# Optimization experiments

Measured on AMD Instinct MI355X. Metric: run time of the kernel, lower is better.

Reference implementation:

```python
import jax, jax.numpy as jnp
import numpy as np
from jax import lax

B, N, C = 4, 16384, 384
HEADS, HD = 8, 48
ALPHA = 4.0
KS = 5
HH = WW = 128


def setup_inputs() -> dict:
    key = jax.random.key(0)
    ks = jax.random.split(key, 9)
    s = 0.02
    return {
        "x": jax.random.normal(ks[0], (B, N, C), jnp.float32),
        "W_qg": jax.random.normal(ks[1], (C, 2 * C), jnp.float32) * s,
        "W_kv": jax.random.normal(ks[2], (C, 2 * C), jnp.float32) * s,
        "W_proj": jax.random.normal(ks[3], (C, C), jnp.float32) * s,
        "b_proj": jnp.zeros((C,), jnp.float32),
        "pos_enc": jax.random.normal(ks[4], (1, N, C), jnp.float32) * 0.02,
        "power_p": jax.random.normal(ks[5], (1, HEADS, 1, HD), jnp.float32) * 0.5,
        "scale_p": jax.random.normal(ks[6], (1, 1, C), jnp.float32) * 0.5,
        "dwc_w": jax.random.normal(ks[7], (HD, 1, KS, KS), jnp.float32) * s,
        "dwc_b": jnp.zeros((HD,), jnp.float32),
        "H": HH,
        "W": WW,
    }


def _relu_pow(x, p):
    # relu(x) ** p with safe gradients at x <= 0
    r = jax.nn.relu(x)
    base = jnp.where(r > 0, r, 1.0)
    return jnp.where(r > 0, base ** p, 0.0)


def reference(x, W_qg, W_kv, W_proj, b_proj, pos_enc, power_p, scale_p, dwc_w, dwc_b, H, W):
    Bx, Nx, Cx = x.shape
    h = power_p.shape[1]
    hd = power_p.shape[-1]

    qg = x @ W_qg                      # [B,N,2C]
    q, g = qg[..., :Cx], qg[..., Cx:]
    kv = x @ W_kv                      # [B,N,2C] (sr_ratio == 1)
    k, v = kv[..., :Cx], kv[..., Cx:]
    n = Nx
    k = k + pos_enc

    scale = jax.nn.softplus(scale_p)            # [1,1,C]
    power = 1.0 + ALPHA * jax.nn.sigmoid(power_p)  # [1,h,1,hd]
    q = q / scale
    k = k / scale

    # [B,h,N,hd]
    q = q.reshape(Bx, Nx, h, hd).transpose(0, 2, 1, 3)
    k = k.reshape(Bx, n, h, hd).transpose(0, 2, 1, 3)
    v = v.reshape(Bx, n, h, hd).transpose(0, 2, 1, 3)

    q_pos = _relu_pow(q, power)
    q_neg = _relu_pow(-q, power)
    k_pos = _relu_pow(k, power)
    k_neg = _relu_pow(-k, power)

    q_sim = jnp.concatenate([q_pos, q_neg], axis=-1)   # [B,h,N,2hd]
    q_opp = jnp.concatenate([q_neg, q_pos], axis=-1)
    kk = jnp.concatenate([k_pos, k_neg], axis=-1)      # [B,h,n,2hd]
    v1, v2 = v[..., : hd // 2], v[..., hd // 2:]

    k_mean = kk.mean(axis=2, keepdims=True)            # [B,h,1,2hd]
    inv_n = 1.0 / n

    z_sim = 1.0 / (jnp.sum(q_sim * k_mean, axis=-1, keepdims=True) + 1e-6)
    kv1 = jnp.einsum('bhnd,bhne->bhde', kk, v1) * inv_n  # [B,h,2hd,hd/2]
    x_sim = jnp.einsum('bhnd,bhde->bhne', q_sim, kv1) * z_sim

    z_opp = 1.0 / (jnp.sum(q_opp * k_mean, axis=-1, keepdims=True) + 1e-6)
    kv2 = jnp.einsum('bhnd,bhne->bhde', kk, v2) * inv_n
    x_opp = jnp.einsum('bhnd,bhde->bhne', q_opp, kv2) * z_opp

    out = jnp.concatenate([x_sim, x_opp], axis=-1)     # [B,h,N,hd]
    out = out.transpose(0, 2, 1, 3).reshape(Bx, Nx, Cx)

    # depthwise conv gate on v
    v4 = v.reshape(Bx * h, H, W, hd).transpose(0, 3, 1, 2)  # [B*h, hd, H, W]
    vc = lax.conv_general_dilated(
        v4, dwc_w, window_strides=(1, 1), padding='SAME',
        feature_group_count=hd,
        dimension_numbers=('NCHW', 'OIHW', 'NCHW'))
    vc = vc + dwc_b[None, :, None, None]
    v_out = vc.reshape(Bx, Cx, Nx).transpose(0, 2, 1)  # [B,N,C]

    out = (out + v_out) * g
    out = out @ W_proj + b_proj
    return out
```

## Files before the change

### kernel.cpp

```cpp
#include <hip/hip_runtime.h>
#include <math.h>


#define NB 4
#define NTOK 16384
#define CDIM 384
#define NHEAD 8
#define HDIM 48
#define IMGH 128
#define IMGW 128

typedef unsigned short u16;
typedef unsigned int u32;
typedef __attribute__((ext_vector_type(8))) short bf16x8;
typedef __attribute__((ext_vector_type(4))) float f32x4;

__device__ __forceinline__ float bf2f(u16 u) {
  return __uint_as_float(((unsigned)u) << 16);
}
__device__ __forceinline__ u16 f2bf(float f) {
  unsigned u = __float_as_uint(f);
  u += 0x7FFF + ((u >> 16) & 1);
  return (u16)(u >> 16);
}
__device__ __forceinline__ float pow_mag(float r, float p) {
  if (r < 1e-20f) return 0.0f;
  return exp2f(fminf(p * log2f(r), 80.0f));
}
__device__ __forceinline__ float ldx1(const void* p, size_t i, bool f32) {
  return f32 ? ((const float*)p)[i] : bf2f(((const u16*)p)[i]);
}
__device__ __forceinline__ void gload16(u16* lds, const u16* g) {
  __builtin_amdgcn_global_load_lds(
      (const __attribute__((address_space(1))) u32*)g,
      (__attribute__((address_space(3))) u32*)lds, 16, 0, 0);
}

__global__ __launch_bounds__(256) void k0_detect(const void* __restrict__ x,
                                                 int* __restrict__ flag) {
  __shared__ int s[256];
  const u16* p = (const u16*)x;
  const int t = threadIdx.x;
  int good = 0;
#pragma unroll
  for (int i = 0; i < 16; ++i) {
    const u16 w = p[t * 16 + i];
    const int e = (w >> 7) & 0xFF;
    good += (e >= 0x60 && e <= 0x85) ? 1 : 0;
  }
  s[t] = good;
  __syncthreads();
  for (int o = 128; o > 0; o >>= 1) {
    if (t < o) s[t] += s[t + o];
    __syncthreads();
  }
  if (t == 0) *flag = (s[0] >= (4096 * 4) / 5) ? 0 : 1;
}

__global__ __launch_bounds__(256) void kx_convert(const void* __restrict__ x,
                                                  const int* __restrict__ flag,
                                                  u16* __restrict__ xbf) {
  if (*flag == 0) return;
  const size_t S = (size_t)NB * NTOK * CDIM;
  const size_t tid = (size_t)blockIdx.x * 256 + threadIdx.x;
  const size_t stride = (size_t)gridDim.x * 256;
  const float4* xf = (const float4*)x;
  for (size_t i = tid; i < S / 8; i += stride) {
    const float4 a = xf[i * 2 + 0];
    const float4 b = xf[i * 2 + 1];
    *(ushort4*)(xbf + i * 8 + 0) = make_ushort4(f2bf(a.x), f2bf(a.y), f2bf(a.z), f2bf(a.w));
    *(ushort4*)(xbf + i * 8 + 4) = make_ushort4(f2bf(b.x), f2bf(b.y), f2bf(b.z), f2bf(b.w));
  }
}

__global__ __launch_bounds__(256) void kprep(
    const void* __restrict__ Wqg, const void* __restrict__ Wkv,
    const void* __restrict__ Wp, const int* __restrict__ flag,
    u16* __restrict__ W2T, u16* __restrict__ WpT)
{
  const bool f32 = (*flag != 0);
  const int idx = blockIdx.x * 256 + threadIdx.x;
  if (idx < 1536 * 384) {
    const int n = idx / 384, k = idx - n * 384;
    const float v = (n < 768) ? ldx1(Wqg, (size_t)k * 768 + n, f32)
                              : ldx1(Wkv, (size_t)k * 768 + (n - 768), f32);
    W2T[idx] = f2bf(v);
  } else {
    const int j = idx - 1536 * 384;
    if (j < 384 * 384) {
      const int n = j / 384, k = j - n * 384;
      WpT[j] = f2bf(ldx1(Wp, (size_t)k * 384 + n, f32));
    }
  }
}

__global__ __launch_bounds__(512) void k1_mfma(
    const void* __restrict__ x, const u16* __restrict__ xbf,
    const u16* __restrict__ W2T,
    const void* __restrict__ pos_enc, const void* __restrict__ scale_p,
    const int* __restrict__ flag, const int conv_ok,
    u16* __restrict__ qsT, u16* __restrict__ gT, u16* __restrict__ ksT, u16* __restrict__ vT)
{
  const bool f32 = (*flag != 0);
  const bool fast = (!f32) || (conv_ok != 0);
  const u16* Asrc = f32 ? xbf : (const u16*)x;
  __shared__ __align__(16) u16 smem[17408];
  u16* Asm = smem;
  u16* Bsm = smem + 8192;
  const int t = threadIdx.x;
  const int bid = blockIdx.x;
  const int rm = (bid & 7) * 768 + (bid >> 3);
  const int m_idx = rm / 12;
  const int n_idx = rm - m_idx * 12;
  const int n0 = n_idx * 128;
  const int m0 = m_idx * 128;
  const int wave = t >> 6, lane = t & 63;
  const int wr = wave >> 2, wc = wave & 3;
  const int lm = lane & 15, lq = lane >> 4;

  f32x4 acc[4][2] = {};

  auto STAGE = [&](int k0) {
#pragma unroll
    for (int i = 0; i < 2; ++i) {
      const int chunk = i * 512 + t;
      const int row = chunk >> 3, c8 = chunk & 7;
      const int sc8 = c8 ^ (row & 7);
      u16* lpA = &Asm[(i * 512 + wave * 64) * 8];
      u16* lpB = &Bsm[(i * 512 + wave * 64) * 8];
      gload16(lpA, Asrc + (size_t)(m0 + row) * CDIM + k0 + sc8 * 8);
      gload16(lpB, W2T + (size_t)(n0 + row) * CDIM + k0 + sc8 * 8);
    }
  };
  auto COMPUTE = [&]() {
#pragma unroll
    for (int kh = 0; kh < 2; ++kh) {
      bf16x8 af[4], bfr[2];
#pragma unroll
      for (int r = 0; r < 4; ++r) {
        const int row = wr * 64 + r * 16 + lm;
        af[r] = *(const bf16x8*)&Asm[row * 64 + (((kh * 4 + lq) ^ (row & 7)) * 8)];
      }
#pragma unroll
      for (int cb = 0; cb < 2; ++cb) {
        const int row = wc * 32 + cb * 16 + lm;
        bfr[cb] = *(const bf16x8*)&Bsm[row * 64 + (((kh * 4 + lq) ^ (row & 7)) * 8)];
      }
#pragma unroll
      for (int r = 0; r < 4; ++r)
#pragma unroll
        for (int cb = 0; cb < 2; ++cb)
          acc[r][cb] = __builtin_amdgcn_mfma_f32_16x16x32_bf16(af[r], bfr[cb], acc[r][cb], 0, 0, 0);
    }
  };

  if (fast) {
    for (int ks = 0; ks < 6; ++ks) {
      STAGE(ks * 64);
      __syncthreads();
      COMPUTE();
      __syncthreads();
    }
  } else {
    for (int k0 = 0; k0 < CDIM; k0 += 64) {
#pragma unroll
      for (int i = 0; i < 2; ++i) {
        const int chunk = t + i * 512;
        const int row = chunk >> 3, c8 = chunk & 7;
        const int ldsoff = row * 64 + ((c8 ^ (row & 7)) * 8);
        const float* xp = (const float*)x + (size_t)(m0 + row) * CDIM + k0 + c8 * 8;
        const float4 v0 = *(const float4*)xp;
        const float4 v1 = *(const float4*)(xp + 4);
        *(ushort4*)&Asm[ldsoff]     = make_ushort4(f2bf(v0.x), f2bf(v0.y), f2bf(v0.z), f2bf(v0.w));
        *(ushort4*)&Asm[ldsoff + 4] = make_ushort4(f2bf(v1.x), f2bf(v1.y), f2bf(v1.z), f2bf(v1.w));
        *(uint4*)&Bsm[ldsoff] = *(const uint4*)(W2T + (size_t)(n0 + row) * CDIM + k0 + c8 * 8);
      }
      __syncthreads();
      COMPUTE();
      __syncthreads();
    }
  }

  u16* et = smem;
  const int b = m0 >> 14;
  const int TOK0 = m0 & (NTOK - 1);
  const int region = n0 / CDIM;
#pragma unroll
  for (int cb = 0; cb < 2; ++cb) {
    const int cl = wc * 32 + cb * 16 + lm;
    const int c = (n0 - region * CDIM) + cl;
    float inv = 1.0f;
    if (region == 0 || region == 2) inv = 1.0f / log1pf(expf(ldx1(scale_p, c, f32)));
#pragma unroll
    for (int r = 0; r < 4; ++r) {
      const int tl = wr * 64 + r * 16 + lq * 4;
      const f32x4 v = acc[r][cb];
      ushort4 w;
      if (region == 2) {
        const int tok = TOK0 + tl;
        const float p0 = ldx1(pos_enc, (size_t)(tok + 0) * CDIM + c, f32);
        const float p1 = ldx1(pos_enc, (size_t)(tok + 1) * CDIM + c, f32);
        const float p2 = ldx1(pos_enc, (size_t)(tok + 2) * CDIM + c, f32);
        const float p3 = ldx1(pos_enc, (size_t)(tok + 3) * CDIM + c, f32);
        w = make_ushort4(f2bf((v[0] + p0) * inv), f2bf((v[1] + p1) * inv),
                         f2bf((v[2] + p2) * inv), f2bf((v[3] + p3) * inv));
      } else if (region == 0) {
        w = make_ushort4(f2bf(v[0] * inv), f2bf(v[1] * inv), f2bf(v[2] * inv), f2bf(v[3] * inv));
      } else {
        w = make_ushort4(f2bf(v[0]), f2bf(v[1]), f2bf(v[2]), f2bf(v[3]));
      }
      *(ushort4*)&et[cl * 136 + tl] = w;
    }
  }
  __syncthreads();
  u16* dst = (region == 0) ? qsT : (region == 1) ? gT : (region == 2) ? ksT : vT;
  const int cbase = b * CDIM + (n0 - region * CDIM);
#pragma unroll
  for (int i = 0; i < 4; ++i) {
    const int idx = i * 512 + t;
    const int row = idx >> 4, seg = idx & 15;
    const uint4 val = *(const uint4*)&et[row * 136 + seg * 8];
    *(uint4*)(dst + ((size_t)(cbase + row)) * NTOK + TOK0 + seg * 8) = val;
  }
}

__global__ __launch_bounds__(256) void k2_stats(
    const u16* __restrict__ ksT, const u16* __restrict__ vT,
    const void* __restrict__ power_p, const int* __restrict__ flag,
    float* __restrict__ km, float* __restrict__ kvm)
{
  const bool f32 = (*flag != 0);
  __shared__ float kkL[96][65];
  __shared__ float vL[48][65];
  __shared__ float pw[48];
  const int bh = blockIdx.x;
  const int b = bh >> 3, h = bh & 7;
  const int t = threadIdx.x;
  if (t < 48) pw[t] = 1.0f + 4.0f / (1.0f + expf(-ldx1(power_p, h * HDIM + t, f32)));
  __syncthreads();
  const int td = t & 15, te = t >> 4;
  float acc[6][3] = {};
  float ksum = 0.0f;
  const u16* ksbase = ksT + ((size_t)(b * CDIM + h * HDIM)) * NTOK;
  const u16* vbase  = vT  + ((size_t)(b * CDIM + h * HDIM)) * NTOK;
  const int n0base = blockIdx.y * 1024;
  for (int tile = 0; tile < 16; ++tile) {
    const int n0 = n0base + tile * 64;
    for (int i = t; i < 48 * 16; i += 256) {
      const int c = i >> 4, qd = (i & 15) * 4;
      ushort4 kq = *(const ushort4*)(ksbase + (size_t)c * NTOK + n0 + qd);
      ushort4 vq = *(const ushort4*)(vbase  + (size_t)c * NTOK + n0 + qd);
      const float p = pw[c];
      float kf[4] = {bf2f(kq.x), bf2f(kq.y), bf2f(kq.z), bf2f(kq.w)};
      float vf[4] = {bf2f(vq.x), bf2f(vq.y), bf2f(vq.z), bf2f(vq.w)};
#pragma unroll
      for (int jj = 0; jj < 4; ++jj) {
        const float f = pow_mag(fabsf(kf[jj]), p);
        kkL[c][qd + jj]      = (kf[jj] > 0.f) ? f : 0.f;
        kkL[c + 48][qd + jj] = (kf[jj] < 0.f) ? f : 0.f;
        vL[c][qd + jj] = vf[jj];
      }
    }
    __syncthreads();
#pragma unroll 2
    for (int nn = 0; nn < 64; ++nn) {
      float av[6], bv[3];
#pragma unroll
      for (int i = 0; i < 6; ++i) av[i] = kkL[td * 6 + i][nn];
#pragma unroll
      for (int j = 0; j < 3; ++j) bv[j] = vL[te * 3 + j][nn];
#pragma unroll
      for (int i = 0; i < 6; ++i)
#pragma unroll
        for (int j = 0; j < 3; ++j)
          acc[i][j] = fmaf(av[i], bv[j], acc[i][j]);
    }
    if (t < 96) {
#pragma unroll 4
      for (int nn = 0; nn < 64; ++nn) ksum += kkL[t][nn];
    }
    __syncthreads();
  }
  const float inv_n = 1.0f / (float)NTOK;
#pragma unroll
  for (int i = 0; i < 6; ++i)
#pragma unroll
    for (int j = 0; j < 3; ++j)
      atomicAdd(&kvm[(size_t)bh * 96 * 48 + (td * 6 + i) * 48 + (te * 3 + j)], acc[i][j] * inv_n);
  if (t < 96) atomicAdd(&km[bh * 96 + t], ksum * inv_n);
}

__global__ __launch_bounds__(256) void k3_attn(
    const u16* __restrict__ qsT, u16* __restrict__ attnT,
    const float* __restrict__ km_g, const float* __restrict__ kvm_g,
    const void* __restrict__ power_p, const int* __restrict__ flag)
{
  const bool f32 = (*flag != 0);
  __shared__ __align__(16) float kvmL[96][48];
  __shared__ float kmL[96];
  __shared__ float pw[48];
  const int bh = blockIdx.y;
  const int b = bh >> 3, h = bh & 7;
  const int t = threadIdx.x;
  for (int i = t; i < 96 * 48; i += 256) kvmL[i / 48][i % 48] = kvm_g[(size_t)bh * 96 * 48 + i];
  if (t < 96) kmL[t] = km_g[bh * 96 + t];
  if (t < 48) pw[t] = 1.0f + 4.0f / (1.0f + expf(-ldx1(power_p, h * HDIM + t, f32)));
  __syncthreads();
  const int n = blockIdx.x * 512 + t;
  const size_t chan0 = ((size_t)(b * CDIM + h * HDIM)) * NTOK + n;
  const u16* qbase = qsT + chan0;
  u16* obase = attnT + chan0;
  float4 accs[2][6] = {}, acco[2][6] = {};
  float zs[2] = {}, zo[2] = {};
  for (int d = 0; d < 48; ++d) {
    const float p = pw[d];
    float qp[2], qn[2];
#pragma unroll
    for (int i = 0; i < 2; ++i) {
      const float qv = bf2f(qbase[(size_t)d * NTOK + i * 256]);
      const float f = pow_mag(fabsf(qv), p);
      qp[i] = (qv > 0.f) ? f : 0.f;
      qn[i] = (qv < 0.f) ? f : 0.f;
      zs[i] = fmaf(qp[i], kmL[d], zs[i]); zs[i] = fmaf(qn[i], kmL[d + 48], zs[i]);
      zo[i] = fmaf(qn[i], kmL[d], zo[i]); zo[i] = fmaf(qp[i], kmL[d + 48], zo[i]);
    }
#pragma unroll
    for (int e4 = 0; e4 < 6; ++e4) {
      const float4 kvA = *(const float4*)&kvmL[d][e4 * 4];
      const float4 kvB = *(const float4*)&kvmL[d + 48][e4 * 4];
      const float4 kvC = *(const float4*)&kvmL[d][24 + e4 * 4];
      const float4 kvD = *(const float4*)&kvmL[d + 48][24 + e4 * 4];
#pragma unroll
      for (int i = 0; i < 2; ++i) {
        accs[i][e4].x = fmaf(qp[i], kvA.x, fmaf(qn[i], kvB.x, accs[i][e4].x));
        accs[i][e4].y = fmaf(qp[i], kvA.y, fmaf(qn[i], kvB.y, accs[i][e4].y));
        accs[i][e4].z = fmaf(qp[i], kvA.z, fmaf(qn[i], kvB.z, accs[i][e4].z));
        accs[i][e4].w = fmaf(qp[i], kvA.w, fmaf(qn[i], kvB.w, accs[i][e4].w));
        acco[i][e4].x = fmaf(qn[i], kvC.x, fmaf(qp[i], kvD.x, acco[i][e4].x));
        acco[i][e4].y = fmaf(qn[i], kvC.y, fmaf(qp[i], kvD.y, acco[i][e4].y));
        acco[i][e4].z = fmaf(qn[i], kvC.z, fmaf(qp[i], kvD.z, acco[i][e4].z));
        acco[i][e4].w = fmaf(qn[i], kvC.w, fmaf(qp[i], kvD.w, acco[i][e4].w));
      }
    }
  }
#pragma unroll
  for (int i = 0; i < 2; ++i) {
    const float zsi = 1.0f / (zs[i] + 1e-6f);
    const float zoi = 1.0f / (zo[i] + 1e-6f);
#pragma unroll
    for (int e4 = 0; e4 < 6; ++e4) {
      const float4 s = accs[i][e4], o = acco[i][e4];
      obase[(size_t)(e4 * 4 + 0) * NTOK + i * 256]    = f2bf(s.x * zsi);
      obase[(size_t)(e4 * 4 + 1) * NTOK + i * 256]    = f2bf(s.y * zsi);
      obase[(size_t)(e4 * 4 + 2) * NTOK + i * 256]    = f2bf(s.z * zsi);
      obase[(size_t)(e4 * 4 + 3) * NTOK + i * 256]    = f2bf(s.w * zsi);
      obase[(size_t)(24 + e4 * 4 + 0) * NTOK + i * 256] = f2bf(o.x * zoi);
      obase[(size_t)(24 + e4 * 4 + 1) * NTOK + i * 256] = f2bf(o.y * zoi);
      obase[(size_t)(24 + e4 * 4 + 2) * NTOK + i * 256] = f2bf(o.z * zoi);
      obase[(size_t)(24 + e4 * 4 + 3) * NTOK + i * 256] = f2bf(o.w * zoi);
    }
  }
}

__global__ __launch_bounds__(256) void k4_conv_combine(
    const u16* __restrict__ vT, const u16* __restrict__ gT,
    const void* __restrict__ dwc_w, const void* __restrict__ dwc_b,
    const int* __restrict__ flag,
    u16* __restrict__ attnT)
{
  const bool f32 = (*flag != 0);
  __shared__ float tile[20][128];
  const int bc = blockIdx.y;
  const int y0 = blockIdx.x * 16;
  const int t = threadIdx.x;
  const int d = bc % 48;
  float w[25];
#pragma unroll
  for (int i = 0; i < 25; ++i) w[i] = ldx1(dwc_w, d * 25 + i, f32);
  const float bias = ldx1(dwc_b, d, f32);
  const u16* vimg = vT + (size_t)bc * NTOK;
  for (int i = t; i < 20 * 128; i += 256) {
    const int r = i >> 7, xx = i & 127;
    const int gy = y0 + r - 2;
    tile[r][xx] = (gy >= 0 && gy < IMGH) ? bf2f(vimg[gy * IMGW + xx]) : 0.f;
  }
  __syncthreads();
  u16* abase = attnT + (size_t)bc * NTOK;
  const u16* gbase = gT + (size_t)bc * NTOK;
#pragma unroll
  for (int k = 0; k < 8; ++k) {
    const int px = t + k * 256;
    const int yy = px >> 7, xcol = px & 127;
    float acc = bias;
#pragma unroll
    for (int dy = 0; dy < 5; ++dy)
#pragma unroll
      for (int dx = 0; dx < 5; ++dx) {
        const int ux = xcol + dx - 2;
        const float val = (ux >= 0 && ux < IMGW) ? tile[yy + dy][ux] : 0.f;
        acc = fmaf(w[dy * 5 + dx], val, acc);
      }
    const int gidx = (y0 + yy) * IMGW + xcol;
    abase[gidx] = f2bf((bf2f(abase[gidx]) + acc) * bf2f(gbase[gidx]));
  }
}

__global__ __launch_bounds__(256) void k4b_transpose(
    const u16* __restrict__ src,
    u16* __restrict__ dst)
{
  __shared__ u16 tile[64][68];
  const int b  = blockIdx.z;
  const int c0 = blockIdx.y * 64;
  const int n0 = blockIdx.x * 64;
  const int t = threadIdx.x;
  const int tr = t >> 4, tq = t & 15;
#pragma unroll
  for (int i = 0; i < 4; ++i) {
    const int r = tr + i * 16;
    *(ushort4*)&tile[r][tq * 4] =
        *(const ushort4*)(src + ((size_t)(b * CDIM + c0 + r)) * NTOK + n0 + tq * 4);
  }
  __syncthreads();
#pragma unroll
  for (int i = 0; i < 4; ++i) {
    const int n = tr + i * 16;
    const ushort4 vv = make_ushort4(tile[tq * 4 + 0][n], tile[tq * 4 + 1][n],
                                    tile[tq * 4 + 2][n], tile[tq * 4 + 3][n]);
    *(ushort4*)(dst + ((size_t)(b * NTOK + n0 + n)) * CDIM + c0 + tq * 4) = vv;
  }
}

__global__ __launch_bounds__(256) void k5_mfma(
    const u16* __restrict__ A,
    const u16* __restrict__ WpT,
    const void* __restrict__ bp, const int* __restrict__ flag,
    void* __restrict__ out)
{
  const bool f32 = (*flag != 0);
  __shared__ __align__(16) u16 Asm[128 * 64];
  __shared__ __align__(16) u16 Bsm[128 * 64];
  const int t = threadIdx.x;
  const int bid = blockIdx.x;
  const int rm = (bid & 7) * 192 + (bid >> 3);
  const int m_idx = rm / 3;
  const int n_idx = rm - m_idx * 3;
  const int n0 = n_idx * 128;
  const int m0 = m_idx * 128;
  const int wave = t >> 6, lane = t & 63;
  const int wr = wave >> 1, wc = wave & 1;
  const int lm = lane & 15, lq = lane >> 4;

  f32x4 acc[4][4] = {};

  auto STAGE = [&](int k0) {
#pragma unroll
    for (int i = 0; i < 4; ++i) {
      const int chunk = i * 256 + t;
      const int row = chunk >> 3, c8 = chunk & 7;
      const int sc8 = c8 ^ (row & 7);
      u16* lpA = &Asm[(i * 256 + wave * 64) * 8];
      u16* lpB = &Bsm[(i * 256 + wave * 64) * 8];
      gload16(lpA, A + (size_t)(m0 + row) * CDIM + k0 + sc8 * 8);
      gload16(lpB, WpT + (size_t)(n0 + row) * CDIM + k0 + sc8 * 8);
    }
  };
  auto COMPUTE = [&]() {
#pragma unroll
    for (int kh = 0; kh < 2; ++kh) {
      bf16x8 af[4], bfr[4];
#pragma unroll
      for (int r = 0; r < 4; ++r) {
        const int row = wr * 64 + r * 16 + lm;
        af[r] = *(const bf16x8*)&Asm[row * 64 + (((kh * 4 + lq) ^ (row & 7)) * 8)];
      }
#pragma unroll
      for (int cb = 0; cb < 4; ++cb) {
        const int row = wc * 64 + cb * 16 + lm;
        bfr[cb] = *(const bf16x8*)&Bsm[row * 64 + (((kh * 4 + lq) ^ (row & 7)) * 8)];
      }
#pragma unroll
      for (int r = 0; r < 4; ++r)
#pragma unroll
        for (int cb = 0; cb < 4; ++cb)
          acc[r][cb] = __builtin_amdgcn_mfma_f32_16x16x32_bf16(af[r], bfr[cb], acc[r][cb], 0, 0, 0);
    }
  };

  for (int ks = 0; ks < 6; ++ks) {
    STAGE(ks * 64);
    __syncthreads();
    COMPUTE();
    __syncthreads();
  }

#pragma unroll
  for (int cb = 0; cb < 4; ++cb) {
    const int cg = n0 + wc * 64 + cb * 16 + lm;
    const float bb = ldx1(bp, cg, f32);
#pragma unroll
    for (int r = 0; r < 4; ++r) {
      const int rowtok = m0 + wr * 64 + r * 16 + lq * 4;
      const f32x4 v = acc[r][cb];
#pragma unroll
      for (int reg = 0; reg < 4; ++reg) {
        const size_t o = (size_t)(rowtok + reg) * CDIM + cg;
        if (f32) ((float*)out)[o] = v[reg] + bb;
        else     ((u16*)out)[o]   = f2bf(v[reg] + bb);
      }
    }
  }
}

extern "C" void kernel_launch(void* const* d_in, const int* in_sizes, int n_in,
                              void* d_out, int out_size, void* d_ws, size_t ws_size,
                              hipStream_t stream) {
  const void* x       = d_in[0];
  const void* Wqg     = d_in[1];
  const void* Wkv     = d_in[2];
  const void* Wproj   = d_in[3];
  const void* bproj   = d_in[4];
  const void* pos_enc = d_in[5];
  const void* power_p = d_in[6];
  const void* scale_p = d_in[7];
  const void* dwc_w   = d_in[8];
  const void* dwc_b   = d_in[9];

  const size_t S = (size_t)NB * NTOK * CDIM;
  const size_t stats_off   = 256;
  const size_t stats_bytes = (size_t)(32 * 96 + 32 * 96 * 48) * sizeof(float);
  const size_t w2t_elems = 1536 * 384, wpt_elems = 384 * 384;
  const size_t need = stats_off + stats_bytes + 3 * S * sizeof(u16)
                    + (w2t_elems + wpt_elems) * sizeof(u16);
  if (ws_size < need) return;

  int*   flag = (int*)d_ws;
  float* km   = (float*)((char*)d_ws + stats_off);
  float* kvm  = km + 32 * 96;
  u16* qsT = (u16*)((char*)d_ws + stats_off + stats_bytes);
  u16* gT  = qsT + S;
  u16* ksT = gT + S;
  u16* W2T = ksT + S;
  u16* WpT = W2T + w2t_elems;
  u16* vT  = (u16*)d_out;

  const int conv_ok = (out_size >= (int)(S * 4)) ? 1 : 0;
  u16* xbf = conv_ok ? ((u16*)d_out + S) : (u16*)d_out;

  hipMemsetAsync(km, 0, stats_bytes, stream);

  k0_detect<<<1, 256, 0, stream>>>(x, flag);
  if (conv_ok) kx_convert<<<2048, 256, 0, stream>>>(x, flag, xbf);
  kprep<<<(int)((w2t_elems + wpt_elems + 255) / 256), 256, 0, stream>>>(
      Wqg, Wkv, Wproj, flag, W2T, WpT);
  k1_mfma<<<6144, 512, 0, stream>>>(x, xbf, W2T, pos_enc, scale_p, flag, conv_ok,
                                    qsT, gT, ksT, vT);
  k2_stats<<<dim3(32, 16), 256, 0, stream>>>(ksT, vT, power_p, flag, km, kvm);
  k3_attn<<<dim3(32, 32), 256, 0, stream>>>(qsT, ksT, km, kvm, power_p, flag);
  k4_conv_combine<<<dim3(8, 1536), 256, 0, stream>>>(vT, gT, dwc_w, dwc_b, flag, ksT);
  k4b_transpose<<<dim3(256, 6, 4), 256, 0, stream>>>(ksT, qsT);
  k5_mfma<<<1536, 256, 0, stream>>>(qsT, WpT, bproj, flag, d_out);
}
```

Before: 794.6 us.

## Double-buffer LDS in projection GEMM and stage fp32 epilogue through shared memory

The output projection GEMM kernel now uses two LDS buffers, so the global-to-LDS loads for the next K slice are issued before computing the current slice, with one barrier per step instead of two. The fp32 epilogue writes accumulators into a padded LDS tile and then stores coalesced float4 rows, replacing scattered scalar stores. This doubles LDS use per block, which may reduce occupancy, and only this last kernel of the pipeline is affected.

```diff
diff --git a/kernel.cpp b/kernel.cpp
--- a/kernel.cpp
+++ b/kernel.cpp
@@ -438,8 +438,11 @@
     void* __restrict__ out)
 {
   const bool f32 = (*flag != 0);
-  __shared__ __align__(16) u16 Asm[128 * 64];
-  __shared__ __align__(16) u16 Bsm[128 * 64];
+  __shared__ __align__(16) u16 smem[32768];
+  u16* Asm0 = smem;
+  u16* Asm1 = smem + 8192;
+  u16* Bsm0 = smem + 16384;
+  u16* Bsm1 = smem + 24576;
   const int t = threadIdx.x;
   const int bid = blockIdx.x;
   const int rm = (bid & 7) * 192 + (bid >> 3);
@@ -453,31 +456,35 @@
 
   f32x4 acc[4][4] = {};
 
-  auto STAGE = [&](int k0) {
+  auto STAGE = [&](int buf, int k0) {
+    u16* Ab = buf ? Asm1 : Asm0;
+    u16* Bb = buf ? Bsm1 : Bsm0;
 #pragma unroll
     for (int i = 0; i < 4; ++i) {
       const int chunk = i * 256 + t;
       const int row = chunk >> 3, c8 = chunk & 7;
       const int sc8 = c8 ^ (row & 7);
-      u16* lpA = &Asm[(i * 256 + wave * 64) * 8];
-      u16* lpB = &Bsm[(i * 256 + wave * 64) * 8];
+      u16* lpA = &Ab[(i * 256 + wave * 64) * 8];
+      u16* lpB = &Bb[(i * 256 + wave * 64) * 8];
       gload16(lpA, A + (size_t)(m0 + row) * CDIM + k0 + sc8 * 8);
       gload16(lpB, WpT + (size_t)(n0 + row) * CDIM + k0 + sc8 * 8);
     }
   };
-  auto COMPUTE = [&]() {
+  auto COMPUTE = [&](int buf) {
+    u16* Ab = buf ? Asm1 : Asm0;
+    u16* Bb = buf ? Bsm1 : Bsm0;
 #pragma unroll
     for (int kh = 0; kh < 2; ++kh) {
       bf16x8 af[4], bfr[4];
 #pragma unroll
       for (int r = 0; r < 4; ++r) {
         const int row = wr * 64 + r * 16 + lm;
-        af[r] = *(const bf16x8*)&Asm[row * 64 + (((kh * 4 + lq) ^ (row & 7)) * 8)];
+        af[r] = *(const bf16x8*)&Ab[row * 64 + (((kh * 4 + lq) ^ (row & 7)) * 8)];
       }
 #pragma unroll
       for (int cb = 0; cb < 4; ++cb) {
         const int row = wc * 64 + cb * 16 + lm;
-        bfr[cb] = *(const bf16x8*)&Bsm[row * 64 + (((kh * 4 + lq) ^ (row & 7)) * 8)];
+        bfr[cb] = *(const bf16x8*)&Bb[row * 64 + (((kh * 4 + lq) ^ (row & 7)) * 8)];
       }
 #pragma unroll
       for (int r = 0; r < 4; ++r)
@@ -487,26 +494,67 @@
     }
   };
 
-  for (int ks = 0; ks < 6; ++ks) {
-    STAGE(ks * 64);
-    __syncthreads();
-    COMPUTE();
-    __syncthreads();
-  }
-
-#pragma unroll
-  for (int cb = 0; cb < 4; ++cb) {
-    const int cg = n0 + wc * 64 + cb * 16 + lm;
-    const float bb = ldx1(bp, cg, f32);
-#pragma unroll
-    for (int r = 0; r < 4; ++r) {
-      const int rowtok = m0 + wr * 64 + r * 16 + lq * 4;
-      const f32x4 v = acc[r][cb];
-#pragma unroll
-      for (int reg = 0; reg < 4; ++reg) {
-        const size_t o = (size_t)(rowtok + reg) * CDIM + cg;
-        if (f32) ((float*)out)[o] = v[reg] + bb;
-        else     ((u16*)out)[o]   = f2bf(v[reg] + bb);
+  STAGE(0, 0);
+  asm volatile("s_waitcnt vmcnt(0)" ::: "memory");
+  __builtin_amdgcn_sched_barrier(0);
+  __builtin_amdgcn_s_barrier();
+  int cur = 0;
+#pragma unroll
+  for (int ks = 0; ks < 5; ++ks) {
+    STAGE(cur ^ 1, (ks + 1) * 64);
+    COMPUTE(cur);
+    asm volatile("s_waitcnt vmcnt(0)" ::: "memory");
+    __builtin_amdgcn_sched_barrier(0);
+    __builtin_amdgcn_s_barrier();
+    cur ^= 1;
+  }
+  COMPUTE(cur);
+
+  if (f32) {
+    float* ef = (float*)smem;
+    float bb[4];
+#pragma unroll
+    for (int cb = 0; cb < 4; ++cb) bb[cb] = ((const float*)bp)[n0 + wc * 64 + cb * 16 + lm];
+    for (int h = 0; h < 2; ++h) {
+      __syncthreads();
+      if (wr == h) {
+#pragma unroll
+        for (int cb = 0; cb < 4; ++cb) {
+          const int cl = wc * 64 + cb * 16 + lm;
+#pragma unroll
+          for (int r = 0; r < 4; ++r) {
+            const int tl = r * 16 + lq * 4;
+            const f32x4 v = acc[r][cb];
+#pragma unroll
+            for (int reg = 0; reg < 4; ++reg)
+              ef[(tl + reg) * 132 + cl] = v[reg] + bb[cb];
+          }
+        }
+      }
+      __syncthreads();
+      float* ob = (float*)out + (size_t)(m0 + h * 64) * CDIM + n0;
+#pragma unroll
+      for (int i = 0; i < 8; ++i) {
+        const int idx = i * 256 + t;
+        const int row = idx >> 5, seg = idx & 31;
+        const float4 val = *(const float4*)&ef[row * 132 + seg * 4];
+        *(float4*)(ob + (size_t)row * CDIM + seg * 4) = val;
+      }
+    }
+  } else {
+#pragma unroll
+    for (int cb = 0; cb < 4; ++cb) {
+      const int cg = n0 + wc * 64 + cb * 16 + lm;
+      const float bbs = bf2f(((const u16*)bp)[cg]);
+#pragma unroll
+      for (int r = 0; r < 4; ++r) {
+        const int rowtok = m0 + wr * 64 + r * 16 + lq * 4;
+        const f32x4 v = acc[r][cb];
+#pragma unroll
+        for (int reg = 0; reg < 4; ++reg) {
+          const size_t o = (size_t)(rowtok + reg) * CDIM + cg;
+          ((u16*)out)[o] = f2bf(v[reg] + bbs);
+        }
       }
     }
   }
```

New measurement: 796.1 us. About the same (+0.2%).
